# Performance work log

Hardware: AMD Instinct MI355X
Metric: run time of the kernel (lower is better)

## Reference

```python
import jax, jax.numpy as jnp
import numpy as np

N_NODES = 100000


def _sage_conv(x, src, dst, wn, ws, b):
    # mean-aggregate neighbor messages at destination nodes
    msgs = x[src]                                        # [E, D] gather
    agg = jax.ops.segment_sum(msgs, dst, num_segments=N_NODES)
    deg = jax.ops.segment_sum(jnp.ones((src.shape[0],), x.dtype), dst,
                              num_segments=N_NODES)
    agg = agg / jnp.maximum(deg, 1.0)[:, None]
    return agg @ wn + x @ ws + b


def setup_inputs() -> dict:
    key = jax.random.key(0)
    k = jax.random.split(key, 5)
    D = 128
    E = 1600000
    EL = 200000
    return {
        "node_features": jax.random.normal(k[0], (N_NODES, D), jnp.float32),
        "edge_index": jax.random.randint(k[1], (2, E), 0, N_NODES, jnp.int64),
        "edge_label_index": jax.random.randint(k[2], (2, EL), 0, N_NODES, jnp.int64),
        "w_neigh": jax.random.normal(k[3], (3, D, D), jnp.float32) * (1.0 / np.sqrt(D)),
        "w_self": jax.random.normal(k[4], (3, D, D), jnp.float32) * (1.0 / np.sqrt(D)),
        "bias": jnp.zeros((3, D), jnp.float32),
    }


def reference(node_features, edge_index, edge_label_index, w_neigh, w_self, bias):
    src, dst = edge_index[0], edge_index[1]
    # layer 0: conv -> relu (dropout is identity in eval mode)
    h = _sage_conv(node_features, src, dst, w_neigh[0], w_self[0], bias[0])
    h = jax.nn.relu(h)
    # middle layer: conv + residual -> relu
    h = jax.nn.relu(_sage_conv(h, src, dst, w_neigh[1], w_self[1], bias[1]) + h)
    # last layer: conv + residual (hidden_dim == output_dim, no projection)
    h = _sage_conv(h, src, dst, w_neigh[2], w_self[2], bias[2]) + h
    # dot-product link decoder
    logits = jnp.sum(h[edge_label_index[0]] * h[edge_label_index[1]], axis=-1)
    return logits
```

## Files before the change

### kernel.cpp

```cpp
#include <hip/hip_runtime.h>
#include <cstdint>
#include <cstddef>

#define D 128

typedef _Float16 half8 __attribute__((ext_vector_type(8)));
typedef float f32x4 __attribute__((ext_vector_type(4)));

static __device__ __forceinline__ unsigned short f2h_bits(float f) {
    union { _Float16 h; unsigned short u; } c;
    c.h = (_Float16)f;
    return c.u;
}

__global__ void hist_kernel(const int* __restrict__ dst, int E,
                            int* __restrict__ counts) {
    int i = blockIdx.x * blockDim.x + threadIdx.x;
    if (i < E) atomicAdd(&counts[dst[i]], 1);
}

__global__ void block_sum_kernel(const int* __restrict__ counts, int n,
                                 int* __restrict__ bsum) {
    __shared__ int sh[256];
    int t = threadIdx.x;
    int i = blockIdx.x * 256 + t;
    sh[t] = (i < n) ? counts[i] : 0;
    __syncthreads();
    for (int off = 128; off; off >>= 1) {
        if (t < off) sh[t] += sh[t + off];
        __syncthreads();
    }
    if (t == 0) bsum[blockIdx.x] = sh[0];
}

__global__ void scan_small_kernel(int* __restrict__ bsum, int nb,
                                  int* __restrict__ row_ptr, int N, int E) {
    __shared__ int sh[512];
    int t = threadIdx.x;
    int v = (t < nb) ? bsum[t] : 0;
    sh[t] = v;
    __syncthreads();
    for (int off = 1; off < 512; off <<= 1) {
        int add = (t >= off) ? sh[t - off] : 0;
        __syncthreads();
        sh[t] += add;
        __syncthreads();
    }
    if (t < nb) bsum[t] = sh[t] - v;
    if (t == 0) row_ptr[N] = E;
}

__global__ void block_scan_kernel(const int* __restrict__ counts, int n,
                                  const int* __restrict__ bsum,
                                  int* __restrict__ row_ptr) {
    __shared__ int sh[256];
    int t = threadIdx.x;
    int i = blockIdx.x * 256 + t;
    int v = (i < n) ? counts[i] : 0;
    sh[t] = v;
    __syncthreads();
    for (int off = 1; off < 256; off <<= 1) {
        int add = (t >= off) ? sh[t - off] : 0;
        __syncthreads();
        sh[t] += add;
        __syncthreads();
    }
    if (i < n) row_ptr[i] = bsum[blockIdx.x] + sh[t] - v;
}

__global__ void fill_kernel(const int* __restrict__ src,
                            const int* __restrict__ dst, int E,
                            const int* __restrict__ row_ptr,
                            int* __restrict__ counts,
                            int* __restrict__ csr_src) {
    int i = blockIdx.x * blockDim.x + threadIdx.x;
    if (i < E) {
        int d = dst[i];
        int pos = row_ptr[d] + atomicSub(&counts[d], 1) - 1;
        csr_src[pos] = src[i];
    }
}

__global__ void f32_to_f16(const float* __restrict__ in,
                           unsigned short* __restrict__ out, int n8) {
    int i = blockIdx.x * 256 + threadIdx.x;
    if (i >= n8) return;
    float4 f0 = ((const float4*)in)[2 * i];
    float4 f1 = ((const float4*)in)[2 * i + 1];
    union { unsigned short u[8]; uint4 v; } o;
    o.u[0] = f2h_bits(f0.x); o.u[1] = f2h_bits(f0.y);
    o.u[2] = f2h_bits(f0.z); o.u[3] = f2h_bits(f0.w);
    o.u[4] = f2h_bits(f1.x); o.u[5] = f2h_bits(f1.y);
    o.u[6] = f2h_bits(f1.z); o.u[7] = f2h_bits(f1.w);
    ((uint4*)out)[i] = o.v;
}

__global__ __launch_bounds__(256) void gather_agg16(
    const unsigned short* __restrict__ h16, const int* __restrict__ row_ptr,
    const int* __restrict__ csr_src,
    unsigned short* __restrict__ agg16, int N) {
    int node = (int)((blockIdx.x * (size_t)blockDim.x + threadIdx.x) >> 6);
    int lane = threadIdx.x & 63;
    if (node >= N) return;
    int beg = row_ptr[node], end = row_ptr[node + 1];
    const int col = lane * 2;
    float ax[8], ay[8];
#pragma unroll
    for (int j = 0; j < 8; j++) { ax[j] = 0.f; ay[j] = 0.f; }
    int e = beg;
    for (; e + 8 <= end; e += 8) {
        int s[8];
#pragma unroll
        for (int j = 0; j < 8; j++) s[j] = csr_src[e + j];
        unsigned int v[8];
#pragma unroll
        for (int j = 0; j < 8; j++)
            v[j] = *(const unsigned int*)(h16 + (size_t)s[j] * D + col);
#pragma unroll
        for (int j = 0; j < 8; j++) {
            union { unsigned int u; _Float16 h[2]; } c; c.u = v[j];
            ax[j] += (float)c.h[0];
            ay[j] += (float)c.h[1];
        }
    }
    for (; e < end; ++e) {
        int s = csr_src[e];
        union { unsigned int u; _Float16 h[2]; } c;
        c.u = *(const unsigned int*)(h16 + (size_t)s * D + col);
        ax[0] += (float)c.h[0];
        ay[0] += (float)c.h[1];
    }
    float sx = (ax[0] + ax[1]) + (ax[2] + ax[3]) + (ax[4] + ax[5]) + (ax[6] + ax[7]);
    float sy = (ay[0] + ay[1]) + (ay[2] + ay[3]) + (ay[4] + ay[5]) + (ay[6] + ay[7]);
    float sc = 1.0f / fmaxf((float)(end - beg), 1.0f);
    union { unsigned int u; _Float16 h[2]; } o;
    o.h[0] = (_Float16)(sx * sc);
    o.h[1] = (_Float16)(sy * sc);
    *(unsigned int*)(agg16 + (size_t)node * D + col) = o.u;
}

__global__ void wprep_kernel(const float* __restrict__ wn,
                             const float* __restrict__ wsf,
                             unsigned short* __restrict__ whp,
                             unsigned short* __restrict__ wlp) {
    int tid = blockIdx.x * 256 + threadIdx.x;
    if (tid >= 12288) return;
    int lane = tid & 63;
    int kb = (tid >> 6) & 7;
    int nb = (tid >> 9) & 7;
    int L  = tid >> 12;
    int n = nb * 16 + (lane & 15);
    int kbase = kb * 32 + (lane >> 4) * 8;
    union { unsigned short u[8]; uint4 v; } oh, ol;
#pragma unroll
    for (int j = 0; j < 8; j++) {
        int k = kbase + j;
        float w = (k < 128) ? wn[L * 16384 + k * 128 + n]
                            : wsf[L * 16384 + (k - 128) * 128 + n];
        _Float16 hi = (_Float16)w;
        _Float16 lo = (_Float16)(w - (float)hi);
        union { _Float16 h; unsigned short u; } ch, cl;
        ch.h = hi; cl.h = lo;
        oh.u[j] = ch.u;
        ol.u[j] = cl.u;
    }
    ((uint4*)whp)[tid] = oh.v;
    ((uint4*)wlp)[tid] = ol.v;
}

template <bool RELU, bool RES, bool F32OUT>
__global__ __launch_bounds__(256) void gemm_mfma16(
    const unsigned short* __restrict__ agg16,
    const unsigned short* __restrict__ h16self,
    const unsigned short* __restrict__ res16,
    const unsigned short* __restrict__ whp,
    const unsigned short* __restrict__ wlp,
    const float* __restrict__ bias,
    float* __restrict__ hout,
    unsigned short* __restrict__ h16out,
    int N) {
    const int t = threadIdx.x;
    const int wv = t >> 6;
    const int lane = t & 63;
    const int r = lane & 15;
    const int q = lane >> 4;
    const int m0 = blockIdx.x * 128 + (wv >> 1) * 64;
    const int nhalf = wv & 1;

    int rowA[4];
#pragma unroll
    for (int mt = 0; mt < 4; mt++) {
        int rr = m0 + mt * 16 + r;
        rowA[mt] = (rr < N) ? rr : (N - 1);
    }

    const unsigned short* whL = whp + lane * 8;
    const unsigned short* wlL = wlp + lane * 8;

    f32x4 acc[4][4];
#pragma unroll
    for (int mt = 0; mt < 4; mt++)
#pragma unroll
        for (int nt = 0; nt < 4; nt++) acc[mt][nt] = (f32x4){0.f, 0.f, 0.f, 0.f};

    half8 aC[4], aN[4], whC[4], whN[4], wlC[4], wlN[4];

    {
        const int ko = q * 8;
#pragma unroll
        for (int mt = 0; mt < 4; mt++)
            aC[mt] = *(const half8*)(agg16 + (size_t)rowA[mt] * D + ko);
#pragma unroll
        for (int nt = 0; nt < 4; nt++) {
            const size_t wo = (size_t)(((nhalf * 4 + nt) * 8 + 0) << 9);
            whC[nt] = *(const half8*)(whL + wo);
            wlC[nt] = *(const half8*)(wlL + wo);
        }
    }

#pragma unroll
    for (int kb = 0; kb < 8; kb++) {
        if (kb < 7) {
            const unsigned short* nbase = ((kb + 1) < 4) ? agg16 : h16self;
            const int ko = ((kb + 1) & 3) * 32 + q * 8;
#pragma unroll
            for (int mt = 0; mt < 4; mt++)
                aN[mt] = *(const half8*)(nbase + (size_t)rowA[mt] * D + ko);
#pragma unroll
            for (int nt = 0; nt < 4; nt++) {
                const size_t wo = (size_t)(((nhalf * 4 + nt) * 8 + (kb + 1)) << 9);
                whN[nt] = *(const half8*)(whL + wo);
                wlN[nt] = *(const half8*)(wlL + wo);
            }
        }
#pragma unroll
        for (int nt = 0; nt < 4; nt++) {
#pragma unroll
            for (int mt = 0; mt < 4; mt++) {
                acc[mt][nt] = __builtin_amdgcn_mfma_f32_16x16x32_f16(
                    aC[mt], whC[nt], acc[mt][nt], 0, 0, 0);
                acc[mt][nt] = __builtin_amdgcn_mfma_f32_16x16x32_f16(
                    aC[mt], wlC[nt], acc[mt][nt], 0, 0, 0);
            }
        }
        if (kb < 7) {
#pragma unroll
            for (int mt = 0; mt < 4; mt++) aC[mt] = aN[mt];
#pragma unroll
            for (int nt = 0; nt < 4; nt++) { whC[nt] = whN[nt]; wlC[nt] = wlN[nt]; }
        }
    }

#pragma unroll
    for (int nt = 0; nt < 4; nt++) {
        const int col = nhalf * 64 + nt * 16 + r;
        const float bv = bias[col];
#pragma unroll
        for (int mt = 0; mt < 4; mt++) {
#pragma unroll
            for (int reg = 0; reg < 4; reg++) {
                int row = m0 + mt * 16 + q * 4 + reg;
                if (row >= N) continue;
                float o = acc[mt][nt][reg] + bv;
                if (RES)
                    o += (float)(*(const _Float16*)(res16 + (size_t)row * D + col));
                if (RELU) o = fmaxf(o, 0.f);
                if (F32OUT) hout[(size_t)row * D + col] = o;
                else        h16out[(size_t)row * D + col] = f2h_bits(o);
            }
        }
    }
}

__global__ void decoder_kernel(const float* __restrict__ h,
                               const int* __restrict__ eli, int EL,
                               float* __restrict__ out) {
    long long tid = (long long)blockIdx.x * blockDim.x + threadIdx.x;
    int lane = (int)(tid & 31);
    long long e = tid >> 5;
    if (e >= EL) return;
    int u = eli[e];
    int v = eli[e + EL];
    float4 a = *(const float4*)(h + (long long)u * D + lane * 4);
    float4 b = *(const float4*)(h + (long long)v * D + lane * 4);
    float p = a.x * b.x + a.y * b.y + a.z * b.z + a.w * b.w;
#pragma unroll
    for (int off = 16; off; off >>= 1) p += __shfl_xor(p, off);
    if (lane == 0) out[e] = p;
}

static inline size_t align256(size_t x) { return (x + 255) & ~(size_t)255; }

extern "C" void kernel_launch(void* const* d_in, const int* in_sizes, int n_in,
                              void* d_out, int out_size, void* d_ws,
                              size_t ws_size, hipStream_t stream) {
    const float* x    = (const float*)d_in[0];
    const int*   ei   = (const int*)d_in[1];
    const int*   eli  = (const int*)d_in[2];
    const float* wn   = (const float*)d_in[3];
    const float* wsf  = (const float*)d_in[4];
    const float* bias = (const float*)d_in[5];

    const int N  = in_sizes[0] / D;
    const int E  = in_sizes[1] / 2;
    const int EL = in_sizes[2] / 2;

    const int* src = ei;
    const int* dst = ei + E;

    char* p = (char*)d_ws;
    int*   counts  = (int*)p;   p += align256((size_t)N * sizeof(int));
    int*   row_ptr = (int*)p;   p += align256((size_t)(N + 1) * sizeof(int));
    int*   bsum    = (int*)p;   p += align256((size_t)1024 * sizeof(int));
    unsigned short* whp = (unsigned short*)p; p += align256((size_t)3 * 32768 * 2);
    unsigned short* wlp = (unsigned short*)p; p += align256((size_t)3 * 32768 * 2);
    int*   csr_src = (int*)p;   p += align256((size_t)E * sizeof(int));
    unsigned short* x16   = (unsigned short*)p; p += align256((size_t)N * D * 2);
    unsigned short* h1    = (unsigned short*)p; p += align256((size_t)N * D * 2);
    unsigned short* h2    = (unsigned short*)p; p += align256((size_t)N * D * 2);
    unsigned short* agg16 = (unsigned short*)p; p += align256((size_t)N * D * 2);
    float* hA      = (float*)p;

    const int nb = (N + 255) / 256;
    const int eb = (E + 255) / 256;
    const int tile_blocks = (N + 127) / 128;
    const int gather_blocks = (N + 3) / 4;
    const int n8 = N * D / 8;

    wprep_kernel<<<48, 256, 0, stream>>>(wn, wsf, whp, wlp);
    f32_to_f16<<<(n8 + 255) / 256, 256, 0, stream>>>(x, x16, n8);

    hipMemsetAsync(counts, 0, (size_t)N * sizeof(int), stream);
    hist_kernel<<<eb, 256, 0, stream>>>(dst, E, counts);
    block_sum_kernel<<<nb, 256, 0, stream>>>(counts, N, bsum);
    scan_small_kernel<<<1, 512, 0, stream>>>(bsum, nb, row_ptr, N, E);
    block_scan_kernel<<<nb, 256, 0, stream>>>(counts, N, bsum, row_ptr);
    fill_kernel<<<eb, 256, 0, stream>>>(src, dst, E, row_ptr, counts, csr_src);

    gather_agg16<<<gather_blocks, 256, 0, stream>>>(x16, row_ptr, csr_src, agg16, N);
    gemm_mfma16<true, false, false><<<tile_blocks, 256, 0, stream>>>(
        agg16, x16, nullptr, whp + 0 * 32768, wlp + 0 * 32768, bias + 0 * D,
        nullptr, h1, N);

    gather_agg16<<<gather_blocks, 256, 0, stream>>>(h1, row_ptr, csr_src, agg16, N);
    gemm_mfma16<true, true, false><<<tile_blocks, 256, 0, stream>>>(
        agg16, h1, h1, whp + 1 * 32768, wlp + 1 * 32768, bias + 1 * D,
        nullptr, h2, N);

    gather_agg16<<<gather_blocks, 256, 0, stream>>>(h2, row_ptr, csr_src, agg16, N);
    gemm_mfma16<false, true, true><<<tile_blocks, 256, 0, stream>>>(
        agg16, h2, h2, whp + 2 * 32768, wlp + 2 * 32768, bias + 2 * D,
        hA, nullptr, N);

    decoder_kernel<<<(int)(((long long)EL * 32 + 255) / 256), 256, 0, stream>>>(
        hA, eli, EL, (float*)d_out);
}
```

Before: 658.8 us.

## Build CSR via two-level bucket sort with shared-memory atomics

```diff
diff --git a/kernel.cpp b/kernel.cpp
--- a/kernel.cpp
+++ b/kernel.cpp
@@ -13,31 +13,29 @@
     return c.u;
 }
 
-__global__ void hist_kernel(const int* __restrict__ dst, int E,
-                            int* __restrict__ counts) {
-    int i = blockIdx.x * blockDim.x + threadIdx.x;
-    if (i < E) atomicAdd(&counts[dst[i]], 1);
-}
-
-__global__ void block_sum_kernel(const int* __restrict__ counts, int n,
-                                 int* __restrict__ bsum) {
-    __shared__ int sh[256];
-    int t = threadIdx.x;
-    int i = blockIdx.x * 256 + t;
-    sh[t] = (i < n) ? counts[i] : 0;
-    __syncthreads();
-    for (int off = 128; off; off >>= 1) {
-        if (t < off) sh[t] += sh[t + off];
-        __syncthreads();
-    }
-    if (t == 0) bsum[blockIdx.x] = sh[0];
-}
-
-__global__ void scan_small_kernel(int* __restrict__ bsum, int nb,
-                                  int* __restrict__ row_ptr, int N, int E) {
+__global__ __launch_bounds__(256) void bucket_hist(
+    const int* __restrict__ dst, int E, int nbkt, int* __restrict__ bcnt) {
+    __shared__ int h[512];
+    const int t = threadIdx.x;
+    for (int i = t; i < nbkt; i += 256) h[i] = 0;
+    __syncthreads();
+    const int base = blockIdx.x * 2048;
+#pragma unroll
+    for (int j = 0; j < 8; j++) {
+        int i = base + j * 256 + t;
+        if (i < E) atomicAdd(&h[dst[i] >> 8], 1);
+    }
+    __syncthreads();
+    for (int i = t; i < nbkt; i += 256)
+        if (h[i]) atomicAdd(&bcnt[i], h[i]);
+}
+
+__global__ void scan_buckets(const int* __restrict__ bcnt, int nbkt,
+                             int* __restrict__ bbase,
+                             int* __restrict__ row_ptr, int N, int E) {
     __shared__ int sh[512];
     int t = threadIdx.x;
-    int v = (t < nb) ? bsum[t] : 0;
+    int v = (t < nbkt) ? bcnt[t] : 0;
     sh[t] = v;
     __syncthreads();
     for (int off = 1; off < 512; off <<= 1) {
@@ -46,17 +44,57 @@
         sh[t] += add;
         __syncthreads();
     }
-    if (t < nb) bsum[t] = sh[t] - v;
+    if (t < nbkt) bbase[t] = sh[t] - v;
+    if (t == 511) bbase[nbkt] = sh[511];
     if (t == 0) row_ptr[N] = E;
 }
 
-__global__ void block_scan_kernel(const int* __restrict__ counts, int n,
-                                  const int* __restrict__ bsum,
-                                  int* __restrict__ row_ptr) {
+__global__ __launch_bounds__(256) void bucket_scatter(
+    const int* __restrict__ src, const int* __restrict__ dst, int E, int nbkt,
+    const int* __restrict__ bbase, int* __restrict__ bcur,
+    unsigned* __restrict__ ebuf) {
+    __shared__ int h[512];
+    __shared__ int bo[512];
+    const int t = threadIdx.x;
+    for (int i = t; i < nbkt; i += 256) h[i] = 0;
+    __syncthreads();
+    const int base = blockIdx.x * 2048;
+    unsigned pk[8]; int bk[8]; int rk[8];
+#pragma unroll
+    for (int j = 0; j < 8; j++) {
+        int i = base + j * 256 + t;
+        bk[j] = -1;
+        if (i < E) {
+            int d = dst[i];
+            bk[j] = d >> 8;
+            pk[j] = (unsigned)src[i] | ((unsigned)(d & 255) << 24);
+            rk[j] = atomicAdd(&h[bk[j]], 1);
+        }
+    }
+    __syncthreads();
+    for (int i = t; i < nbkt; i += 256)
+        bo[i] = h[i] ? atomicAdd(&bcur[i], h[i]) : 0;
+    __syncthreads();
+#pragma unroll
+    for (int j = 0; j < 8; j++)
+        if (bk[j] >= 0)
+            ebuf[bbase[bk[j]] + bo[bk[j]] + rk[j]] = pk[j];
+}
+
+__global__ __launch_bounds__(256) void bucket_fill(
+    const unsigned* __restrict__ ebuf, const int* __restrict__ bbase,
+    int* __restrict__ row_ptr, int* __restrict__ csr_src, int N) {
+    __shared__ int cnt[256];
     __shared__ int sh[256];
-    int t = threadIdx.x;
-    int i = blockIdx.x * 256 + t;
-    int v = (i < n) ? counts[i] : 0;
+    const int t = threadIdx.x;
+    const int bkt = blockIdx.x;
+    const int beg = bbase[bkt], end = bbase[bkt + 1];
+    cnt[t] = 0;
+    __syncthreads();
+    for (int i = beg + t; i < end; i += 256)
+        atomicAdd(&cnt[ebuf[i] >> 24], 1);
+    __syncthreads();
+    int v = cnt[t];
     sh[t] = v;
     __syncthreads();
     for (int off = 1; off < 256; off <<= 1) {
@@ -65,19 +103,16 @@
         sh[t] += add;
         __syncthreads();
     }
-    if (i < n) row_ptr[i] = bsum[blockIdx.x] + sh[t] - v;
-}
-
-__global__ void fill_kernel(const int* __restrict__ src,
-                            const int* __restrict__ dst, int E,
-                            const int* __restrict__ row_ptr,
-                            int* __restrict__ counts,
-                            int* __restrict__ csr_src) {
-    int i = blockIdx.x * blockDim.x + threadIdx.x;
-    if (i < E) {
-        int d = dst[i];
-        int pos = row_ptr[d] + atomicSub(&counts[d], 1) - 1;
-        csr_src[pos] = src[i];
+    const int excl = sh[t] - v;
+    const int node = bkt * 256 + t;
+    if (node < N) row_ptr[node] = beg + excl;
+    __syncthreads();
+    cnt[t] = beg + excl;
+    __syncthreads();
+    for (int i = beg + t; i < end; i += 256) {
+        unsigned p = ebuf[i];
+        int pos = atomicAdd(&cnt[p >> 24], 1);
+        csr_src[pos] = (int)(p & 0xFFFFFFu);
     }
 }
 
@@ -308,12 +343,16 @@
     const int* src = ei;
     const int* dst = ei + E;
 
+    const int nbkt = (N + 255) / 256;
+
     char* p = (char*)d_ws;
-    int*   counts  = (int*)p;   p += align256((size_t)N * sizeof(int));
+    int*   bcnt    = (int*)p;   p += align256((size_t)512 * sizeof(int));
+    int*   bcur    = (int*)p;   p += align256((size_t)512 * sizeof(int));
+    int*   bbase   = (int*)p;   p += align256((size_t)516 * sizeof(int));
     int*   row_ptr = (int*)p;   p += align256((size_t)(N + 1) * sizeof(int));
-    int*   bsum    = (int*)p;   p += align256((size_t)1024 * sizeof(int));
     unsigned short* whp = (unsigned short*)p; p += align256((size_t)3 * 32768 * 2);
     unsigned short* wlp = (unsigned short*)p; p += align256((size_t)3 * 32768 * 2);
+    unsigned* ebuf = (unsigned*)p; p += align256((size_t)E * sizeof(unsigned));
     int*   csr_src = (int*)p;   p += align256((size_t)E * sizeof(int));
     unsigned short* x16   = (unsigned short*)p; p += align256((size_t)N * D * 2);
     unsigned short* h1    = (unsigned short*)p; p += align256((size_t)N * D * 2);
@@ -321,8 +360,7 @@
     unsigned short* agg16 = (unsigned short*)p; p += align256((size_t)N * D * 2);
     float* hA      = (float*)p;
 
-    const int nb = (N + 255) / 256;
-    const int eb = (E + 255) / 256;
+    const int eb2k = (E + 2047) / 2048;
     const int tile_blocks = (N + 127) / 128;
     const int gather_blocks = (N + 3) / 4;
     const int n8 = N * D / 8;
@@ -330,12 +368,11 @@
     wprep_kernel<<<48, 256, 0, stream>>>(wn, wsf, whp, wlp);
     f32_to_f16<<<(n8 + 255) / 256, 256, 0, stream>>>(x, x16, n8);
 
-    hipMemsetAsync(counts, 0, (size_t)N * sizeof(int), stream);
-    hist_kernel<<<eb, 256, 0, stream>>>(dst, E, counts);
-    block_sum_kernel<<<nb, 256, 0, stream>>>(counts, N, bsum);
-    scan_small_kernel<<<1, 512, 0, stream>>>(bsum, nb, row_ptr, N, E);
-    block_scan_kernel<<<nb, 256, 0, stream>>>(counts, N, bsum, row_ptr);
-    fill_kernel<<<eb, 256, 0, stream>>>(src, dst, E, row_ptr, counts, csr_src);
+    hipMemsetAsync(bcnt, 0, (size_t)1024 * sizeof(int), stream);
+    bucket_hist<<<eb2k, 256, 0, stream>>>(dst, E, nbkt, bcnt);
+    scan_buckets<<<1, 512, 0, stream>>>(bcnt, nbkt, bbase, row_ptr, N, E);
+    bucket_scatter<<<eb2k, 256, 0, stream>>>(src, dst, E, nbkt, bbase, bcur, ebuf);
+    bucket_fill<<<nbkt, 256, 0, stream>>>(ebuf, bbase, row_ptr, csr_src, N);
 
     gather_agg16<<<gather_blocks, 256, 0, stream>>>(x16, row_ptr, csr_src, agg16, N);
     gemm_mfma16<true, false, false><<<tile_blocks, 256, 0, stream>>>(
```

Result: faster. 595.9 us (-9.6%).
